# Kernel tuning notes

Measured on AMD Instinct MI355X. Metric: run time of the kernel, lower is better.

The kernel has to match this reference:

```python
import jax, jax.numpy as jnp
import numpy as np

B, T, D, H = 2, 2048, 1024, 16
HD = D // H  # head_dim = 64


def setup_inputs() -> dict:
    key = jax.random.key(0)
    ks = jax.random.split(key, 5)
    s = 0.02
    return {
        "x": jax.random.normal(ks[0], (B, T, D), dtype=jnp.float32),
        "Wqkv": jax.random.normal(ks[1], (3 * D, D), dtype=jnp.float32) * s,
        "bqkv": jax.random.normal(ks[2], (3 * D,), dtype=jnp.float32) * s,
        "Wproj": jax.random.normal(ks[3], (D, D), dtype=jnp.float32) * s,
        "bproj": jax.random.normal(ks[4], (D,), dtype=jnp.float32) * s,
    }


def reference(x, Wqkv, bqkv, Wproj, bproj):
    b, t, d = x.shape
    qkv = x @ Wqkv.T + bqkv                      # [B,T,3D]
    q, k, v = jnp.split(qkv, 3, axis=-1)
    # [B,T,D] -> [B,H,T,HD]
    def to_heads(u):
        return u.reshape(b, t, H, HD).transpose(0, 2, 1, 3)
    q, k, v = to_heads(q), to_heads(k), to_heads(v)
    scale = 1.0 / jnp.sqrt(jnp.float32(HD))
    attn = jnp.einsum("bhqd,bhkd->bhqk", q, k) * scale   # [B,H,T,T]
    causal = jnp.tril(jnp.ones((t, t), dtype=bool))
    attn = jnp.where(causal[None, None, :, :], attn, -jnp.inf)
    attn = jax.nn.softmax(attn, axis=-1)
    scores = jnp.einsum("bhqk,bhkd->bhqd", attn, v)       # [B,H,T,HD]
    scores = scores.transpose(0, 2, 1, 3).reshape(b, t, d)
    return scores @ Wproj.T + bproj
```

## Files before the change

### kernel.cpp

```cpp
#include <hip/hip_runtime.h>

typedef __bf16 bf16_8 __attribute__((ext_vector_type(8)));
typedef __bf16 bf16_4 __attribute__((ext_vector_type(4)));
typedef float  f32_4  __attribute__((ext_vector_type(4)));
typedef short  s16x4  __attribute__((ext_vector_type(4)));

typedef __attribute__((address_space(1))) const void* as1_cvp;
typedef __attribute__((address_space(3))) void*       as3_vp;

__device__ __forceinline__ void load16_to_lds(const void* g, void* l) {
    __builtin_amdgcn_global_load_lds((as1_cvp)g, (as3_vp)l, 16, 0, 0);
}

__device__ __forceinline__ f32_4 mfma16x16x16(bf16_4 a, bf16_4 b, f32_4 c) {
#if __has_builtin(__builtin_amdgcn_mfma_f32_16x16x16_bf16)
    return __builtin_amdgcn_mfma_f32_16x16x16_bf16(a, b, c, 0, 0, 0);
#else
    return __builtin_amdgcn_mfma_f32_16x16x16bf16_1k(
        __builtin_bit_cast(s16x4, a), __builtin_bit_cast(s16x4, b), c, 0, 0, 0);
#endif
}

__global__ __launch_bounds__(256) void cvt_all(
    const float* __restrict__ a, const float* __restrict__ b,
    const float* __restrict__ c, __bf16* __restrict__ out,
    int na4, int nb4, int nc4)
{
    int i = blockIdx.x * 256 + threadIdx.x;
    if (i >= na4 + nb4 + nc4) return;
    float4 f;
    if (i < na4)            f = ((const float4*)a)[i];
    else if (i < na4 + nb4) f = ((const float4*)b)[i - na4];
    else                    f = ((const float4*)c)[i - na4 - nb4];
    bf16_4 v = { (__bf16)f.x, (__bf16)f.y, (__bf16)f.z, (__bf16)f.w };
    ((bf16_4*)out)[i] = v;
}

#define BM 128

template<int OUT_BF16, int BN_, int QKV>
__global__ __launch_bounds__(256) void gemm_bt(
    const __bf16* __restrict__ A,
    const __bf16* __restrict__ B,
    const float*  __restrict__ bias,
    __bf16* __restrict__ Cb, float* __restrict__ Cf,
    __bf16* __restrict__ Vtb,
    int M, int N, int K, int ldc)
{
    constexpr int NT   = BN_ / 32;
    constexpr int CSTR = BN_ + (OUT_BF16 ? 8 : 4);
    __shared__ __align__(16) char smem[35840];
    __bf16* As = (__bf16*)smem;
    __bf16* Bs = As + 128 * 64;

    const int tid  = threadIdx.x;
    const int wave = tid >> 6;
    const int lane = tid & 63;
    const int wm = wave >> 1, wn = wave & 1;
    const int quad = lane >> 4, l16 = lane & 15;
    const int bm = blockIdx.y * BM, bn = blockIdx.x * BN_;

    const int r0 = tid >> 3;
    const int ch = tid & 7;
    const int cs = (ch ^ (r0 & 7)) * 8;

    f32_4 acc[4][NT];
    #pragma unroll
    for (int i = 0; i < 4; ++i)
        #pragma unroll
        for (int j = 0; j < NT; ++j)
            acc[i][j] = f32_4{0.f, 0.f, 0.f, 0.f};

    for (int k0 = 0; k0 < K; k0 += 64) {
        __syncthreads();
        #pragma unroll
        for (int p = 0; p < 4; ++p) {
            int row = p * 32 + r0;
            load16_to_lds(A + (size_t)(bm + row) * K + k0 + cs,
                          &As[(p * 32 + wave * 8) * 64]);
        }
        #pragma unroll
        for (int p = 0; p < BN_ / 32; ++p) {
            int row = p * 32 + r0;
            load16_to_lds(B + (size_t)(bn + row) * K + k0 + cs,
                          &Bs[(p * 32 + wave * 8) * 64]);
        }
        __syncthreads();

        #pragma unroll
        for (int h = 0; h < 2; ++h) {
            const int sl = ((quad + h * 4) ^ (l16 & 7)) * 8;
            bf16_8 af[4], bfr[NT];
            #pragma unroll
            for (int mt = 0; mt < 4; ++mt)
                af[mt] = *(const bf16_8*)&As[(wm * 64 + mt * 16 + l16) * 64 + sl];
            #pragma unroll
            for (int nt = 0; nt < NT; ++nt)
                bfr[nt] = *(const bf16_8*)&Bs[(wn * (BN_/2) + nt * 16 + l16) * 64 + sl];
            #pragma unroll
            for (int mt = 0; mt < 4; ++mt)
                #pragma unroll
                for (int nt = 0; nt < NT; ++nt)
                    acc[mt][nt] = __builtin_amdgcn_mfma_f32_16x16x32_bf16(
                        af[mt], bfr[nt], acc[mt][nt], 0, 0, 0);
        }
    }

    if (QKV && bn >= 2048) {
        const int b_ = bm >> 11;
        const int t0 = (bm & 2047) + wm * 64;
        #pragma unroll
        for (int nt = 0; nt < NT; ++nt) {
            int vrow = (bn - 2048) + wn * (BN_/2) + nt * 16 + l16;
            float bv = bias ? bias[2048 + vrow] : 0.f;
            #pragma unroll
            for (int mt = 0; mt < 4; ++mt) {
                bf16_4 ov;
                #pragma unroll
                for (int r = 0; r < 4; ++r)
                    ov[r] = (__bf16)(acc[mt][nt][r] + bv);
                *(bf16_4*)(Vtb + ((size_t)b_ * 1024 + vrow) * 2048
                           + t0 + mt * 16 + quad * 4) = ov;
            }
        }
        return;
    }

    __syncthreads();

    if (OUT_BF16) {
        __bf16* Cs = (__bf16*)smem;
        #pragma unroll
        for (int mt = 0; mt < 4; ++mt)
            #pragma unroll
            for (int nt = 0; nt < NT; ++nt) {
                int col = wn * (BN_/2) + nt * 16 + l16;
                float bv = bias ? bias[bn + col] : 0.f;
                #pragma unroll
                for (int r = 0; r < 4; ++r)
                    Cs[(wm * 64 + mt * 16 + quad * 4 + r) * CSTR + col] =
                        (__bf16)(acc[mt][nt][r] + bv);
            }
        __syncthreads();
        const int rr = tid >> 4, cc = (tid & 15) * 8;
        #pragma unroll
        for (int p = 0; p < 8; ++p) {
            int row = p * 16 + rr;
            bf16_8 v = *(const bf16_8*)&Cs[row * CSTR + cc];
            *(bf16_8*)(Cb + (size_t)(bm + row) * ldc + bn + cc) = v;
        }
    } else {
        float* Cs = (float*)smem;
        #pragma unroll
        for (int mt = 0; mt < 4; ++mt)
            #pragma unroll
            for (int nt = 0; nt < NT; ++nt) {
                int col = wn * (BN_/2) + nt * 16 + l16;
                float bv = bias ? bias[bn + col] : 0.f;
                #pragma unroll
                for (int r = 0; r < 4; ++r)
                    Cs[(wm * 64 + mt * 16 + quad * 4 + r) * CSTR + col] =
                        acc[mt][nt][r] + bv;
            }
        __syncthreads();
        const int rr = tid >> 4, cc = (tid & 15) * 4;
        #pragma unroll
        for (int p = 0; p < 8; ++p) {
            int row = p * 16 + rr;
            float4 v = *(const float4*)&Cs[row * CSTR + cc];
            *(float4*)(Cf + (size_t)(bm + row) * ldc + bn + cc) = v;
        }
    }
}

__global__ __launch_bounds__(512, 4) void attn_kernel(
    const __bf16* __restrict__ qk, const __bf16* __restrict__ vt,
    __bf16* __restrict__ out)
{
    constexpr int T = 2048;
    __shared__ __align__(16) char pool[35328];
    __bf16* Ks = (__bf16*)pool;
    __bf16* Vt = (__bf16*)(pool + 16384);
    float*  Om = (float*)pool;
    float*  Lm = (float*)(pool + 34816);

    const int tid  = threadIdx.x;
    const int wave = tid >> 6;
    const int lane = tid & 63;
    const int wg = wave >> 2, wq = wave & 3;
    const int quad = lane >> 4, l16 = lane & 15;

    const int fid  = blockIdx.x;
    const int xcd  = fid & 7;
    const int half = fid >> 8;
    const int w    = (fid >> 3) & 31;
    const int qt   = half ? (7 - (w >> 2)) : ((w >> 2) + 8);
    const int bh   = xcd * 4 + (w & 3);
    const int b = bh >> 4, h = bh & 15;
    const int jmax = 2 * qt + 1;

    const size_t rowbase = (size_t)b * T;
    const __bf16* Kbase = qk + 1024 + h * 64;
    const __bf16* Vbase = vt + (size_t)bh * 64 * 2048;

    const int srow = tid >> 3;
    const int sch  = tid & 7;
    const int schf = sch ^ (srow & 7);

    bf16_8 aq[2][2];
    #pragma unroll
    for (int mt = 0; mt < 2; ++mt) {
        const __bf16* qrow =
            qk + (rowbase + qt * 128 + wq * 32 + mt * 16 + l16) * 2048 + h * 64;
        aq[mt][0] = *(const bf16_8*)(qrow + quad * 8);
        aq[mt][1] = *(const bf16_8*)(qrow + 32 + quad * 8);
        #pragma unroll
        for (int u = 0; u < 8; ++u) {
            aq[mt][0][u] = (__bf16)((float)aq[mt][0][u] * 0.125f);
            aq[mt][1][u] = (__bf16)((float)aq[mt][1][u] * 0.125f);
        }
    }

    load16_to_lds(Kbase + (rowbase + srow) * 2048 + schf * 8, &Ks[wave * 512]);
    load16_to_lds(Vbase + (size_t)srow * 2048 + schf * 8,     &Vt[wave * 512]);

    float l_i[2] = {0.f, 0.f};
    f32_4 O[2][4];
    #pragma unroll
    for (int mt = 0; mt < 2; ++mt)
        #pragma unroll
        for (int dt = 0; dt < 4; ++dt) O[mt][dt] = f32_4{0.f, 0.f, 0.f, 0.f};

    for (int j = 0; j <= jmax; ++j) {
        const int cur = j & 1, nxt = cur ^ 1;
        __syncthreads();

        if (j < jmax) {
            const int jn = j + 1;
            load16_to_lds(Kbase + (rowbase + jn * 64 + srow) * 2048 + schf * 8,
                          &Ks[nxt * 4096 + wave * 512]);
            load16_to_lds(Vbase + (size_t)srow * 2048 + jn * 64 + schf * 8,
                          &Vt[nxt * 4096 + wave * 512]);
        }

        f32_4 S[2][2];
        #pragma unroll
        for (int nt = 0; nt < 2; ++nt) {
            int rk = wg * 32 + nt * 16 + l16;
            int rx = rk & 7;
            bf16_8 kb0 = *(const bf16_8*)&Ks[cur * 4096 + rk * 64 + ((quad ^ rx) << 3)];
            bf16_8 kb1 = *(const bf16_8*)&Ks[cur * 4096 + rk * 64 + (((quad + 4) ^ rx) << 3)];
            #pragma unroll
            for (int mt = 0; mt < 2; ++mt) {
                f32_4 zz = {0.f, 0.f, 0.f, 0.f};
                zz = __builtin_amdgcn_mfma_f32_16x16x32_bf16(kb0, aq[mt][0], zz, 0, 0, 0);
                zz = __builtin_amdgcn_mfma_f32_16x16x32_bf16(kb1, aq[mt][1], zz, 0, 0, 0);
                S[mt][nt] = zz;
            }
        }

        const bool diag = (j >= 2 * qt);
        bf16_4 bp[2][2];
        #pragma unroll
        for (int mt = 0; mt < 2; ++mt) {
            int qg = qt * 128 + wq * 32 + mt * 16 + l16;
            #pragma unroll
            for (int nt = 0; nt < 2; ++nt) {
                #pragma unroll
                for (int rr = 0; rr < 4; ++rr) {
                    float p = __expf(S[mt][nt][rr]);
                    if (diag) {
                        int key = j * 64 + wg * 32 + nt * 16 + quad * 4 + rr;
                        if (key > qg) p = 0.f;
                    }
                    l_i[mt] += p;
                    bp[mt][nt][rr] = (__bf16)p;
                }
            }
        }

        #pragma unroll
        for (int dt = 0; dt < 4; ++dt) {
            int d = dt * 16 + l16;
            int dsw = d & 7;
            #pragma unroll
            for (int nt = 0; nt < 2; ++nt) {
                int chv = (wg * 4 + nt * 2 + (quad >> 1)) ^ dsw;
                bf16_4 vaf = *(const bf16_4*)&Vt[cur * 4096 + d * 64 + chv * 8 + (quad & 1) * 4];
                #pragma unroll
                for (int mt = 0; mt < 2; ++mt)
                    O[mt][dt] = mfma16x16x16(vaf, bp[mt][nt], O[mt][dt]);
            }
        }
    }

    float lw[2];
    #pragma unroll
    for (int mt = 0; mt < 2; ++mt) {
        float v = l_i[mt];
        v += __shfl_xor(v, 16, 64);
        v += __shfl_xor(v, 32, 64);
        lw[mt] = v;
    }
    __syncthreads();
    if (wg == 1) {
        #pragma unroll
        for (int mt = 0; mt < 2; ++mt) {
            #pragma unroll
            for (int dt = 0; dt < 4; ++dt)
                *(f32_4*)&Om[(wq * 32 + mt * 16 + l16) * 68 + dt * 16 + quad * 4] = O[mt][dt];
            if (quad == 0) Lm[wq * 32 + mt * 16 + l16] = lw[mt];
        }
    }
    __syncthreads();
    if (wg == 0) {
        #pragma unroll
        for (int mt = 0; mt < 2; ++mt) {
            float inv = 1.f / (lw[mt] + Lm[wq * 32 + mt * 16 + l16]);
            int q = qt * 128 + wq * 32 + mt * 16 + l16;
            #pragma unroll
            for (int dt = 0; dt < 4; ++dt) {
                f32_4 o2 = *(const f32_4*)&Om[(wq * 32 + mt * 16 + l16) * 68 + dt * 16 + quad * 4];
                bf16_4 ov;
                #pragma unroll
                for (int rr = 0; rr < 4; ++rr)
                    ov[rr] = (__bf16)((O[mt][dt][rr] + o2[rr]) * inv);
                *(bf16_4*)(out + (rowbase + q) * 1024 + h * 64 + dt * 16 + quad * 4) = ov;
            }
        }
    }
}

extern "C" void kernel_launch(void* const* d_in, const int* in_sizes, int n_in,
                              void* d_out, int out_size, void* d_ws, size_t ws_size,
                              hipStream_t stream)
{
    constexpr int Bc = 2, Tc = 2048, Dc = 1024;
    constexpr int M  = Bc * Tc;
    constexpr int N1 = 3 * Dc;

    const float* x     = (const float*)d_in[0];
    const float* Wqkv  = (const float*)d_in[1];
    const float* bqkv  = (const float*)d_in[2];
    const float* Wproj = (const float*)d_in[3];
    const float* bproj = (const float*)d_in[4];
    float* outp = (float*)d_out;

    __bf16* xb     = (__bf16*)d_ws;
    __bf16* wqkvb  = xb     + (size_t)M * Dc;
    __bf16* wprojb = wqkvb  + (size_t)N1 * Dc;
    __bf16* qkb    = wprojb + (size_t)Dc * Dc;
    __bf16* vtb    = qkb    + (size_t)M * 2048;
    __bf16* attnb  = vtb    + (size_t)Bc * 1024 * 2048;

    {
        int na4 = M * Dc / 4, nb4 = N1 * Dc / 4, nc4 = Dc * Dc / 4;
        int n4 = na4 + nb4 + nc4;
        cvt_all<<<(n4 + 255) / 256, 256, 0, stream>>>(x, Wqkv, Wproj, xb, na4, nb4, nc4);
    }

    gemm_bt<1, 128, 1><<<dim3(N1 / 128, M / BM), 256, 0, stream>>>(
        xb, wqkvb, bqkv, qkb, nullptr, vtb, M, N1, Dc, 2048);

    attn_kernel<<<dim3(512), 512, 0, stream>>>(qkb, vtb, attnb);

    gemm_bt<0, 64, 0><<<dim3(Dc / 64, M / BM), 256, 0, stream>>>(
        attnb, wprojb, bproj, nullptr, outp, nullptr, M, Dc, Dc, Dc);
}
```

Baseline: 170.2 us.

## Double attention key tile to 128 and stage V-transpose stores through LDS

The attention kernel now processes 128 keys per iteration instead of 64, halving the loop trip count and the number of barriers, with each wave group handling 64 keys. LDS grows to 64 KB for the double-buffered K and V tiles, which may lower occupancy under the 4-block launch bound. Separately, the QKV GEMM epilogue for V writes the transposed tile into shared memory first, then emits coalesced 16-byte rows to global memory instead of scattered 8-byte stores.

After: 172.0 us. About the same (+1.0%).

```diff
diff --git a/kernel.cpp b/kernel.cpp
--- a/kernel.cpp
+++ b/kernel.cpp
@@ -106,27 +106,36 @@
         }
     }
 
+    __syncthreads();
+
     if (QKV && bn >= 2048) {
+        constexpr int VSTR = 136;
+        __bf16* Cs = (__bf16*)smem;
         const int b_ = bm >> 11;
-        const int t0 = (bm & 2047) + wm * 64;
+        const int t0 = bm & 2047;
         #pragma unroll
         for (int nt = 0; nt < NT; ++nt) {
-            int vrow = (bn - 2048) + wn * (BN_/2) + nt * 16 + l16;
-            float bv = bias ? bias[2048 + vrow] : 0.f;
+            int col = wn * (BN_/2) + nt * 16 + l16;
+            float bv = bias ? bias[bn + col] : 0.f;
             #pragma unroll
             for (int mt = 0; mt < 4; ++mt) {
                 bf16_4 ov;
                 #pragma unroll
                 for (int r = 0; r < 4; ++r)
                     ov[r] = (__bf16)(acc[mt][nt][r] + bv);
-                *(bf16_4*)(Vtb + ((size_t)b_ * 1024 + vrow) * 2048
-                           + t0 + mt * 16 + quad * 4) = ov;
-            }
+                *(bf16_4*)&Cs[col * VSTR + wm * 64 + mt * 16 + quad * 4] = ov;
+            }
+        }
+        __syncthreads();
+        const int rr = tid >> 1, hh = tid & 1;
+        #pragma unroll
+        for (int c = 0; c < 8; ++c) {
+            bf16_8 v = *(const bf16_8*)&Cs[rr * VSTR + (hh * 8 + c) * 8];
+            *(bf16_8*)(Vtb + ((size_t)b_ * 1024 + (bn - 2048) + rr) * 2048
+                       + t0 + (hh * 8 + c) * 8) = v;
         }
         return;
     }
-
-    __syncthreads();
 
     if (OUT_BF16) {
         __bf16* Cs = (__bf16*)smem;
@@ -178,9 +187,9 @@
     __bf16* __restrict__ out)
 {
     constexpr int T = 2048;
-    __shared__ __align__(16) char pool[35328];
+    __shared__ __align__(16) char pool[65536];
     __bf16* Ks = (__bf16*)pool;
-    __bf16* Vt = (__bf16*)(pool + 16384);
+    __bf16* Vt = (__bf16*)(pool + 32768);
     float*  Om = (float*)pool;
     float*  Lm = (float*)(pool + 34816);
 
@@ -197,15 +206,14 @@
     const int qt   = half ? (7 - (w >> 2)) : ((w >> 2) + 8);
     const int bh   = xcd * 4 + (w & 3);
     const int b = bh >> 4, h = bh & 15;
-    const int jmax = 2 * qt + 1;
+    const int jmax = qt;
 
     const size_t rowbase = (size_t)b * T;
     const __bf16* Kbase = qk + 1024 + h * 64;
     const __bf16* Vbase = vt + (size_t)bh * 64 * 2048;
 
-    const int srow = tid >> 3;
-    const int sch  = tid & 7;
-    const int schf = sch ^ (srow & 7);
+    const int krow = tid >> 3, kch = tid & 7;
+    const int vd   = tid >> 4, vch = tid & 15;
 
     bf16_8 aq[2][2];
     #pragma unroll
@@ -221,8 +229,15 @@
         }
     }
 
-    load16_to_lds(Kbase + (rowbase + srow) * 2048 + schf * 8, &Ks[wave * 512]);
-    load16_to_lds(Vbase + (size_t)srow * 2048 + schf * 8,     &Vt[wave * 512]);
+    #pragma unroll
+    for (int p = 0; p < 2; ++p) {
+        int r = p * 64 + krow;
+        load16_to_lds(Kbase + (rowbase + r) * 2048 + ((kch ^ (r & 7)) * 8),
+                      &Ks[(p * 64 + wave * 8) * 64]);
+        int d = p * 32 + vd;
+        load16_to_lds(Vbase + (size_t)d * 2048 + ((vch ^ (d & 7)) * 8),
+                      &Vt[(p * 32 + wave * 4) * 128]);
+    }
 
     float l_i[2] = {0.f, 0.f};
     f32_4 O[2][4];
@@ -237,40 +252,36 @@
 
         if (j < jmax) {
             const int jn = j + 1;
-            load16_to_lds(Kbase + (rowbase + jn * 64 + srow) * 2048 + schf * 8,
-                          &Ks[nxt * 4096 + wave * 512]);
-            load16_to_lds(Vbase + (size_t)srow * 2048 + jn * 64 + schf * 8,
-                          &Vt[nxt * 4096 + wave * 512]);
-        }
-
-        f32_4 S[2][2];
-        #pragma unroll
-        for (int nt = 0; nt < 2; ++nt) {
-            int rk = wg * 32 + nt * 16 + l16;
+            #pragma unroll
+            for (int p = 0; p < 2; ++p) {
+                int r = p * 64 + krow;
+                load16_to_lds(Kbase + (rowbase + jn * 128 + r) * 2048 + ((kch ^ (r & 7)) * 8),
+                              &Ks[nxt * 8192 + (p * 64 + wave * 8) * 64]);
+                int d = p * 32 + vd;
+                load16_to_lds(Vbase + (size_t)d * 2048 + jn * 128 + ((vch ^ (d & 7)) * 8),
+                              &Vt[nxt * 8192 + (p * 32 + wave * 4) * 128]);
+            }
+        }
+
+        const bool diag = (j == qt);
+        bf16_4 bp[2][4];
+        #pragma unroll
+        for (int nt = 0; nt < 4; ++nt) {
+            int rk = wg * 64 + nt * 16 + l16;
             int rx = rk & 7;
-            bf16_8 kb0 = *(const bf16_8*)&Ks[cur * 4096 + rk * 64 + ((quad ^ rx) << 3)];
-            bf16_8 kb1 = *(const bf16_8*)&Ks[cur * 4096 + rk * 64 + (((quad + 4) ^ rx) << 3)];
+            bf16_8 kb0 = *(const bf16_8*)&Ks[cur * 8192 + rk * 64 + ((quad ^ rx) << 3)];
+            bf16_8 kb1 = *(const bf16_8*)&Ks[cur * 8192 + rk * 64 + (((quad + 4) ^ rx) << 3)];
             #pragma unroll
             for (int mt = 0; mt < 2; ++mt) {
                 f32_4 zz = {0.f, 0.f, 0.f, 0.f};
                 zz = __builtin_amdgcn_mfma_f32_16x16x32_bf16(kb0, aq[mt][0], zz, 0, 0, 0);
                 zz = __builtin_amdgcn_mfma_f32_16x16x32_bf16(kb1, aq[mt][1], zz, 0, 0, 0);
-                S[mt][nt] = zz;
-            }
-        }
-
-        const bool diag = (j >= 2 * qt);
-        bf16_4 bp[2][2];
-        #pragma unroll
-        for (int mt = 0; mt < 2; ++mt) {
-            int qg = qt * 128 + wq * 32 + mt * 16 + l16;
-            #pragma unroll
-            for (int nt = 0; nt < 2; ++nt) {
+                int qg = qt * 128 + wq * 32 + mt * 16 + l16;
                 #pragma unroll
                 for (int rr = 0; rr < 4; ++rr) {
-                    float p = __expf(S[mt][nt][rr]);
+                    float p = __expf(zz[rr]);
                     if (diag) {
-                        int key = j * 64 + wg * 32 + nt * 16 + quad * 4 + rr;
+                        int key = j * 128 + wg * 64 + nt * 16 + quad * 4 + rr;
                         if (key > qg) p = 0.f;
                     }
                     l_i[mt] += p;
@@ -284,9 +295,10 @@
             int d = dt * 16 + l16;
             int dsw = d & 7;
             #pragma unroll
-            for (int nt = 0; nt < 2; ++nt) {
-                int chv = (wg * 4 + nt * 2 + (quad >> 1)) ^ dsw;
-                bf16_4 vaf = *(const bf16_4*)&Vt[cur * 4096 + d * 64 + chv * 8 + (quad & 1) * 4];
+            for (int nt = 0; nt < 4; ++nt) {
+                int c = wg * 8 + nt * 2 + (quad >> 1);
+                bf16_4 vaf = *(const bf16_4*)&Vt[cur * 8192 + d * 128
+                                                 + ((c ^ dsw) << 3) + (quad & 1) * 4];
                 #pragma unroll
                 for (int mt = 0; mt < 2; ++mt)
                     O[mt][dt] = mfma16x16x16(vaf, bp[mt][nt], O[mt][dt]);
```

## Double-buffer GEMM LDS tiles with K=32 steps and stage V-transpose stores through LDS

Applied to the files above, without the earlier changes.

Replaces the single-buffered K=64 tile loop with a two-stage LDS ring of K=32 tiles, issuing async global-to-LDS loads for the next tile before computing the current one. This cuts one barrier per iteration and is meant to overlap memory latency with MFMA work. The transposed V epilogue now writes through an LDS staging buffer so each thread emits contiguous 16-byte global stores instead of scattered 8-byte ones. In exchange there are twice as many loop iterations, each with half the MFMA work per barrier, and a different swizzle pattern.

Measured after the change: 170.6 us. About the same (+0.2%).

```diff
diff --git a/kernel.cpp b/kernel.cpp
--- a/kernel.cpp
+++ b/kernel.cpp
@@ -49,9 +49,9 @@
 {
     constexpr int NT   = BN_ / 32;
     constexpr int CSTR = BN_ + (OUT_BF16 ? 8 : 4);
-    __shared__ __align__(16) char smem[35840];
+    __shared__ __align__(16) char smem[34816];
     __bf16* As = (__bf16*)smem;
-    __bf16* Bs = As + 128 * 64;
+    __bf16* Bs = (__bf16*)(smem + 16384);
 
     const int tid  = threadIdx.x;
     const int wave = tid >> 6;
@@ -60,9 +60,8 @@
     const int quad = lane >> 4, l16 = lane & 15;
     const int bm = blockIdx.y * BM, bn = blockIdx.x * BN_;
 
-    const int r0 = tid >> 3;
-    const int ch = tid & 7;
-    const int cs = (ch ^ (r0 & 7)) * 8;
+    const int r0 = tid >> 2;
+    const int cf = ((tid & 3) ^ (r0 & 3)) * 8;
 
     f32_4 acc[4][NT];
     #pragma unroll
@@ -71,62 +70,81 @@
         for (int j = 0; j < NT; ++j)
             acc[i][j] = f32_4{0.f, 0.f, 0.f, 0.f};
 
-    for (int k0 = 0; k0 < K; k0 += 64) {
-        __syncthreads();
-        #pragma unroll
-        for (int p = 0; p < 4; ++p) {
-            int row = p * 32 + r0;
-            load16_to_lds(A + (size_t)(bm + row) * K + k0 + cs,
-                          &As[(p * 32 + wave * 8) * 64]);
-        }
-        #pragma unroll
-        for (int p = 0; p < BN_ / 32; ++p) {
-            int row = p * 32 + r0;
-            load16_to_lds(B + (size_t)(bn + row) * K + k0 + cs,
-                          &Bs[(p * 32 + wave * 8) * 64]);
-        }
-        __syncthreads();
-
-        #pragma unroll
-        for (int h = 0; h < 2; ++h) {
-            const int sl = ((quad + h * 4) ^ (l16 & 7)) * 8;
-            bf16_8 af[4], bfr[NT];
-            #pragma unroll
-            for (int mt = 0; mt < 4; ++mt)
-                af[mt] = *(const bf16_8*)&As[(wm * 64 + mt * 16 + l16) * 64 + sl];
+    const int NIT = K >> 5;
+
+    {
+        #pragma unroll
+        for (int p = 0; p < 2; ++p)
+            load16_to_lds(A + (size_t)(bm + p * 64 + r0) * K + cf,
+                          &As[(p * 64 + wave * 16) * 32]);
+        #pragma unroll
+        for (int p = 0; p < BN_ / 64; ++p)
+            load16_to_lds(B + (size_t)(bn + p * 64 + r0) * K + cf,
+                          &Bs[(p * 64 + wave * 16) * 32]);
+    }
+
+    for (int j = 0; j < NIT; ++j) {
+        const int cur = j & 1, nxt = cur ^ 1;
+        __syncthreads();
+
+        if (j + 1 < NIT) {
+            const int k0 = (j + 1) * 32;
+            #pragma unroll
+            for (int p = 0; p < 2; ++p)
+                load16_to_lds(A + (size_t)(bm + p * 64 + r0) * K + k0 + cf,
+                              &As[nxt * 4096 + (p * 64 + wave * 16) * 32]);
+            #pragma unroll
+            for (int p = 0; p < BN_ / 64; ++p)
+                load16_to_lds(B + (size_t)(bn + p * 64 + r0) * K + k0 + cf,
+                              &Bs[nxt * (BN_ * 32) + (p * 64 + wave * 16) * 32]);
+        }
+
+        const int sl = ((quad ^ (l16 & 3)) << 3);
+        bf16_8 af[4], bfr[NT];
+        #pragma unroll
+        for (int mt = 0; mt < 4; ++mt)
+            af[mt] = *(const bf16_8*)&As[cur * 4096 + (wm * 64 + mt * 16 + l16) * 32 + sl];
+        #pragma unroll
+        for (int nt = 0; nt < NT; ++nt)
+            bfr[nt] = *(const bf16_8*)&Bs[cur * (BN_ * 32) + (wn * (BN_/2) + nt * 16 + l16) * 32 + sl];
+        #pragma unroll
+        for (int mt = 0; mt < 4; ++mt)
             #pragma unroll
             for (int nt = 0; nt < NT; ++nt)
-                bfr[nt] = *(const bf16_8*)&Bs[(wn * (BN_/2) + nt * 16 + l16) * 64 + sl];
-            #pragma unroll
-            for (int mt = 0; mt < 4; ++mt)
-                #pragma unroll
-                for (int nt = 0; nt < NT; ++nt)
-                    acc[mt][nt] = __builtin_amdgcn_mfma_f32_16x16x32_bf16(
-                        af[mt], bfr[nt], acc[mt][nt], 0, 0, 0);
-        }
-    }
+                acc[mt][nt] = __builtin_amdgcn_mfma_f32_16x16x32_bf16(
+                    af[mt], bfr[nt], acc[mt][nt], 0, 0, 0);
+    }
+
+    __syncthreads();
 
     if (QKV && bn >= 2048) {
+        constexpr int VSTR = 136;
+        __bf16* Cs = (__bf16*)smem;
         const int b_ = bm >> 11;
-        const int t0 = (bm & 2047) + wm * 64;
+        const int t0 = bm & 2047;
         #pragma unroll
         for (int nt = 0; nt < NT; ++nt) {
-            int vrow = (bn - 2048) + wn * (BN_/2) + nt * 16 + l16;
-            float bv = bias ? bias[2048 + vrow] : 0.f;
+            int col = wn * (BN_/2) + nt * 16 + l16;
+            float bv = bias ? bias[bn + col] : 0.f;
             #pragma unroll
             for (int mt = 0; mt < 4; ++mt) {
                 bf16_4 ov;
                 #pragma unroll
                 for (int r = 0; r < 4; ++r)
                     ov[r] = (__bf16)(acc[mt][nt][r] + bv);
-                *(bf16_4*)(Vtb + ((size_t)b_ * 1024 + vrow) * 2048
-                           + t0 + mt * 16 + quad * 4) = ov;
-            }
+                *(bf16_4*)&Cs[col * VSTR + wm * 64 + mt * 16 + quad * 4] = ov;
+            }
+        }
+        __syncthreads();
+        const int rr = tid >> 1, hh = tid & 1;
+        #pragma unroll
+        for (int c = 0; c < 8; ++c) {
+            bf16_8 v = *(const bf16_8*)&Cs[rr * VSTR + (hh * 8 + c) * 8];
+            *(bf16_8*)(Vtb + ((size_t)b_ * 1024 + (bn - 2048) + rr) * 2048
+                       + t0 + (hh * 8 + c) * 8) = v;
         }
         return;
     }
-
-    __syncthreads();
 
     if (OUT_BF16) {
         __bf16* Cs = (__bf16*)smem;
```
